# Performance work log

Hardware: AMD Instinct MI355X
Metric: run time of the kernel (lower is better)

Reference implementation:

```python
import jax, jax.numpy as jnp
import numpy as np

IN_CH = 12
STEP = 4
UPLAG = 2048
HIDDEN = 1024
OUTPUT = 256
BATCH = 2048
FEAT = UPLAG // STEP  # per-channel conv output length


def setup_inputs() -> dict:
    key = jax.random.key(0)
    ks = jax.random.split(key, 7)
    s = 1.0 / np.sqrt(STEP)
    x = jax.random.normal(ks[0], (BATCH, IN_CH, UPLAG), dtype=jnp.float32)
    # per-channel Conv1d(1,1,step,step) weights/biases, stacked: [C, step], [C]
    W1 = jax.random.uniform(ks[1], (IN_CH, STEP), jnp.float32, -s, s)
    b1 = jax.random.uniform(ks[2], (IN_CH,), jnp.float32, -s, s)
    d_in = IN_CH * FEAT
    s2 = 1.0 / np.sqrt(d_in)
    W2 = jax.random.uniform(ks[3], (d_in, HIDDEN), jnp.float32, -s2, s2)
    b2 = jax.random.uniform(ks[4], (HIDDEN,), jnp.float32, -s2, s2)
    s3 = 1.0 / np.sqrt(HIDDEN)
    W3 = jax.random.uniform(ks[5], (HIDDEN, OUTPUT), jnp.float32, -s3, s3)
    b3 = jax.random.uniform(ks[6], (OUTPUT,), jnp.float32, -s3, s3)
    return {"x": x, "W1": W1, "b1": b1, "W2": W2, "b2": b2, "W3": W3, "b3": b3}


def reference(x, W1, b1, W2, b2, W3, b3):
    B, C, L = x.shape
    # Non-overlapping patch reduction equivalent to Conv1d(1,1,step,step) per channel:
    # view [B, C, F, step], contract step dim against per-channel kernel.
    xp = x.reshape(B, C, L // STEP, STEP)
    conv = jnp.einsum('bcfk,ck->bcf', xp, W1) + b1[None, :, None]  # [B, C, F]
    flat = conv.reshape(B, C * (L // STEP))  # concat order: channel-major, matches torch.cat
    h = jax.nn.relu(flat @ W2 + b2)
    out = h @ W3 + b3
    return out.reshape(B, 1, -1)
```

## Files before the change

kernel.cpp:

```cpp
#include <hip/hip_runtime.h>
#include <hip/hip_bf16.h>

#define BATCH   2048
#define IN_CH   12
#define UPLAG   2048
#define STEP    4
#define FEAT    512
#define DIN     6144
#define HIDDEN  1024
#define OUTPUT  256

typedef __bf16 bf16x8 __attribute__((ext_vector_type(8)));
typedef float  f32x4  __attribute__((ext_vector_type(4)));

__device__ __forceinline__ unsigned short f2bf(float f) {
  unsigned int u = __builtin_bit_cast(unsigned int, f);
  unsigned int r = (u + 0x7fffu + ((u >> 16) & 1u)) >> 16;
  return (unsigned short)r;
}

__device__ __forceinline__ float bf2f(unsigned short h) {
  unsigned int u = ((unsigned int)h) << 16;
  return __builtin_bit_cast(float, u);
}

__device__ __forceinline__ void async_copy16(const unsigned short* g, unsigned short* l) {
  __builtin_amdgcn_global_load_lds(
      (const __attribute__((address_space(1))) unsigned int*)g,
      (__attribute__((address_space(3))) unsigned int*)l, 16, 0, 0);
}

__global__ __launch_bounds__(256) void conv_cast_kernel(
    const float* __restrict__ x, const float* __restrict__ W1,
    const float* __restrict__ b1, unsigned short* __restrict__ out)
{
  int gid = blockIdx.x * 256 + threadIdx.x;
  const int total = BATCH * DIN;
  if (gid >= total) return;
  int cf = gid % DIN;
  int c  = cf >> 9;
  float4 xv = ((const float4*)x)[gid];
  float4 wv = ((const float4*)W1)[c];
  float v = xv.x * wv.x + xv.y * wv.y + xv.z * wv.z + xv.w * wv.w + b1[c];
  out[gid] = f2bf(v);
}

__global__ __launch_bounds__(256) void transpose_cast(
    const float* __restrict__ in, unsigned short* __restrict__ out,
    int R, int Ncol)
{
  __shared__ float tile[32][33];
  int bx = blockIdx.x * 32;
  int by = blockIdx.y * 32;
  int tx = threadIdx.x, ty = threadIdx.y;
  #pragma unroll
  for (int i = 0; i < 32; i += 8)
    tile[ty + i][tx] = in[(size_t)(by + ty + i) * Ncol + bx + tx];
  __syncthreads();
  #pragma unroll
  for (int i = 0; i < 32; i += 8)
    out[(size_t)(bx + ty + i) * R + by + tx] = f2bf(tile[tx][ty + i]);
}

#define G1_BM 128
#define G1_BN 128
#define G1_BK 32
#define SPLITK 6

__global__ __launch_bounds__(256, 2) void gemm1_kernel(
    const unsigned short* __restrict__ A,
    const unsigned short* __restrict__ BT,
    unsigned short* __restrict__ Cp,
    int M, int N, int K)
{
  __shared__ unsigned short As[G1_BM * G1_BK];
  __shared__ unsigned short Bs[G1_BN * G1_BK];
  const int t    = threadIdx.x;
  const int lane = t & 63;
  const int wave = t >> 6;

  int b    = blockIdx.x;
  int xcdg = b & 7;
  int rest = b >> 3;
  int xt   = rest & 7;
  int zz   = rest >> 3;
  int zt   = zz >> 1;
  int yt   = (xcdg << 1) | (zz & 1);

  const int m0 = yt * G1_BM;
  const int n0 = xt * G1_BN;
  const int Ks = K / SPLITK;
  const int kbeg = zt * Ks;

  const int wm = (wave >> 1) * 64;
  const int wn = (wave & 1) * 64;
  const int lm = lane & 15;
  const int lk = (lane >> 4) * 8;

  f32x4 acc[4][4];
  #pragma unroll
  for (int i = 0; i < 4; i++)
    #pragma unroll
    for (int j = 0; j < 4; j++) {
      f32x4 z = {0.f, 0.f, 0.f, 0.f};
      acc[i][j] = z;
    }

  const unsigned short* Ag = A  + (size_t)m0 * K + kbeg;
  const unsigned short* Bg = BT + (size_t)n0 * K + kbeg;

  for (int kk = 0; kk < Ks; kk += G1_BK) {
    #pragma unroll
    for (int r = 0; r < 2; ++r) {
      int chunk = r * 256 + t;
      int row = chunk >> 2;
      int kc  = (chunk & 3) * 8;
      async_copy16(Ag + (size_t)row * K + kk + kc, As + chunk * 8);
    }
    #pragma unroll
    for (int r = 0; r < 2; ++r) {
      int chunk = r * 256 + t;
      int row = chunk >> 2;
      int kc  = (chunk & 3) * 8;
      async_copy16(Bg + (size_t)row * K + kk + kc, Bs + chunk * 8);
    }
    __syncthreads();

    bf16x8 af[4], bfr[4];
    #pragma unroll
    for (int i = 0; i < 4; i++)
      af[i] = *(const bf16x8*)(As + (wm + i * 16 + lm) * G1_BK + lk);
    #pragma unroll
    for (int j = 0; j < 4; j++)
      bfr[j] = *(const bf16x8*)(Bs + (wn + j * 16 + lm) * G1_BK + lk);
    #pragma unroll
    for (int i = 0; i < 4; i++)
      #pragma unroll
      for (int j = 0; j < 4; j++)
        acc[i][j] = __builtin_amdgcn_mfma_f32_16x16x32_bf16(af[i], bfr[j], acc[i][j], 0, 0, 0);
    __syncthreads();
  }

  unsigned short* Co = Cp + (size_t)zt * M * N;
  const int rbase = (lane >> 4) * 4;
  #pragma unroll
  for (int i = 0; i < 4; i++)
    #pragma unroll
    for (int j = 0; j < 4; j++) {
      int col = n0 + wn + j * 16 + lm;
      #pragma unroll
      for (int r = 0; r < 4; r++) {
        int row = m0 + wm + i * 16 + rbase + r;
        Co[(size_t)row * N + col] = f2bf(acc[i][j][r]);
      }
    }
}

__global__ __launch_bounds__(256) void reduce_bias_relu(
    const unsigned short* __restrict__ Cp, const float* __restrict__ b2,
    unsigned short* __restrict__ H)
{
  const int MN = BATCH * HIDDEN;
  int i4 = blockIdx.x * 256 + threadIdx.x;
  if (i4 >= MN / 4) return;
  float4 s = {0.f, 0.f, 0.f, 0.f};
  #pragma unroll
  for (int p = 0; p < SPLITK; ++p) {
    ushort4 a = ((const ushort4*)(Cp + (size_t)p * MN))[i4];
    s.x += bf2f(a.x); s.y += bf2f(a.y); s.z += bf2f(a.z); s.w += bf2f(a.w);
  }
  int col = (i4 * 4) & (HIDDEN - 1);
  float4 bb = *(const float4*)(b2 + col);
  ushort4 o;
  o.x = f2bf(fmaxf(s.x + bb.x, 0.f));
  o.y = f2bf(fmaxf(s.y + bb.y, 0.f));
  o.z = f2bf(fmaxf(s.z + bb.z, 0.f));
  o.w = f2bf(fmaxf(s.w + bb.w, 0.f));
  ((ushort4*)H)[i4] = o;
}

#define SPLITK2 4

__global__ __launch_bounds__(256, 2) void gemm2_kernel(
    const unsigned short* __restrict__ A,
    const unsigned short* __restrict__ BT,
    unsigned short* __restrict__ Cp)
{
  const int M = BATCH, N = OUTPUT, K = HIDDEN;
  __shared__ unsigned short As[64 * 32];
  __shared__ unsigned short Bs[64 * 32];
  const int t    = threadIdx.x;
  const int lane = t & 63;
  const int wave = t >> 6;
  const int m0 = blockIdx.y * 64;
  const int n0 = blockIdx.x * 64;
  const int Ks = K / SPLITK2;
  const int kbeg = blockIdx.z * Ks;
  const int wm = (wave >> 1) * 32;
  const int wn = (wave & 1) * 32;
  const int lm = lane & 15;
  const int lk = (lane >> 4) * 8;
  const int row = t >> 2;
  const int kc  = (t & 3) * 8;

  f32x4 acc[2][2];
  #pragma unroll
  for (int i = 0; i < 2; i++)
    #pragma unroll
    for (int j = 0; j < 2; j++) {
      f32x4 z = {0.f, 0.f, 0.f, 0.f};
      acc[i][j] = z;
    }

  const unsigned short* Ag = A  + (size_t)m0 * K + kbeg;
  const unsigned short* Bg = BT + (size_t)n0 * K + kbeg;

  for (int kk = 0; kk < Ks; kk += 32) {
    async_copy16(Ag + (size_t)row * K + kk + kc, As + t * 8);
    async_copy16(Bg + (size_t)row * K + kk + kc, Bs + t * 8);
    __syncthreads();
    bf16x8 af[2], bfr[2];
    #pragma unroll
    for (int i = 0; i < 2; i++)
      af[i] = *(const bf16x8*)(As + (wm + i * 16 + lm) * 32 + lk);
    #pragma unroll
    for (int j = 0; j < 2; j++)
      bfr[j] = *(const bf16x8*)(Bs + (wn + j * 16 + lm) * 32 + lk);
    #pragma unroll
    for (int i = 0; i < 2; i++)
      #pragma unroll
      for (int j = 0; j < 2; j++)
        acc[i][j] = __builtin_amdgcn_mfma_f32_16x16x32_bf16(af[i], bfr[j], acc[i][j], 0, 0, 0);
    __syncthreads();
  }

  unsigned short* Co = Cp + (size_t)blockIdx.z * M * N;
  const int rbase = (lane >> 4) * 4;
  #pragma unroll
  for (int i = 0; i < 2; i++)
    #pragma unroll
    for (int j = 0; j < 2; j++) {
      int col = n0 + wn + j * 16 + lm;
      #pragma unroll
      for (int r = 0; r < 4; r++) {
        int row_o = m0 + wm + i * 16 + rbase + r;
        Co[(size_t)row_o * N + col] = f2bf(acc[i][j][r]);
      }
    }
}

__global__ __launch_bounds__(256) void reduce2_bias(
    const unsigned short* __restrict__ Cp, const float* __restrict__ b3,
    float* __restrict__ out)
{
  const int MN = BATCH * OUTPUT;
  int i4 = blockIdx.x * 256 + threadIdx.x;
  if (i4 >= MN / 4) return;
  float4 s = {0.f, 0.f, 0.f, 0.f};
  #pragma unroll
  for (int p = 0; p < SPLITK2; ++p) {
    ushort4 a = ((const ushort4*)(Cp + (size_t)p * MN))[i4];
    s.x += bf2f(a.x); s.y += bf2f(a.y); s.z += bf2f(a.z); s.w += bf2f(a.w);
  }
  int col = (i4 * 4) & (OUTPUT - 1);
  float4 bb = *(const float4*)(b3 + col);
  float4 o = {s.x + bb.x, s.y + bb.y, s.z + bb.z, s.w + bb.w};
  ((float4*)out)[i4] = o;
}

extern "C" void kernel_launch(void* const* d_in, const int* in_sizes, int n_in,
                              void* d_out, int out_size, void* d_ws, size_t ws_size,
                              hipStream_t stream)
{
  const float* x  = (const float*)d_in[0];
  const float* W1 = (const float*)d_in[1];
  const float* b1 = (const float*)d_in[2];
  const float* W2 = (const float*)d_in[3];
  const float* b2 = (const float*)d_in[4];
  const float* W3 = (const float*)d_in[5];
  const float* b3 = (const float*)d_in[6];
  float* out = (float*)d_out;

  char* ws = (char*)d_ws;
  unsigned short* flatA = (unsigned short*)ws; ws += (size_t)BATCH * DIN * 2;
  unsigned short* W2T   = (unsigned short*)ws; ws += (size_t)HIDDEN * DIN * 2;
  unsigned short* W3T   = (unsigned short*)ws; ws += (size_t)OUTPUT * HIDDEN * 2;
  unsigned short* Cpart = (unsigned short*)ws; ws += (size_t)SPLITK * BATCH * HIDDEN * 2;
  unsigned short* H     = (unsigned short*)ws; ws += (size_t)BATCH * HIDDEN * 2;
  unsigned short* Cp2   = (unsigned short*)ws; ws += (size_t)SPLITK2 * BATCH * OUTPUT * 2;

  conv_cast_kernel<<<(BATCH * DIN) / 256, 256, 0, stream>>>(x, W1, b1, flatA);
  transpose_cast<<<dim3(HIDDEN / 32, DIN / 32), dim3(32, 8), 0, stream>>>(W2, W2T, DIN, HIDDEN);
  transpose_cast<<<dim3(OUTPUT / 32, HIDDEN / 32), dim3(32, 8), 0, stream>>>(W3, W3T, HIDDEN, OUTPUT);
  gemm1_kernel<<<768, 256, 0, stream>>>(flatA, W2T, Cpart, BATCH, HIDDEN, DIN);
  reduce_bias_relu<<<(BATCH * HIDDEN / 4) / 256, 256, 0, stream>>>(Cpart, b2, H);
  gemm2_kernel<<<dim3(OUTPUT / 64, BATCH / 64, SPLITK2), 256, 0, stream>>>(H, W3T, Cp2);
  reduce2_bias<<<(BATCH * OUTPUT / 4) / 256, 256, 0, stream>>>(Cp2, b3, out);
}
```

Baseline: 350.4 us.

## Fuse prep kernels and use swizzled BK=64 LDS tiles in both GEMMs

Merges the conv/cast and the two weight transpose-casts into one launch, with 64x64 transpose tiles. Both GEMMs double their K tile to 64 and store LDS rows with an XOR swizzle on 16-byte chunks, which halves the number of barrier pairs per K and is meant to cut LDS bank conflicts on fragment reads. LDS per block doubles, which may limit occupancy, and the fused prep kernel has grid-stride conv blocks alongside transpose blocks that use a 64x65 shared tile.

```diff
diff --git a/kernel.cpp b/kernel.cpp
--- a/kernel.cpp
+++ b/kernel.cpp
@@ -30,41 +30,56 @@
       (__attribute__((address_space(3))) unsigned int*)l, 16, 0, 0);
 }
 
-__global__ __launch_bounds__(256) void conv_cast_kernel(
+#define CONV_BLOCKS 4096
+#define W2T_BLOCKS  1536
+#define W3T_BLOCKS  64
+
+__global__ __launch_bounds__(256) void prep_kernel(
     const float* __restrict__ x, const float* __restrict__ W1,
-    const float* __restrict__ b1, unsigned short* __restrict__ out)
-{
-  int gid = blockIdx.x * 256 + threadIdx.x;
-  const int total = BATCH * DIN;
-  if (gid >= total) return;
-  int cf = gid % DIN;
-  int c  = cf >> 9;
-  float4 xv = ((const float4*)x)[gid];
-  float4 wv = ((const float4*)W1)[c];
-  float v = xv.x * wv.x + xv.y * wv.y + xv.z * wv.z + xv.w * wv.w + b1[c];
-  out[gid] = f2bf(v);
-}
-
-__global__ __launch_bounds__(256) void transpose_cast(
-    const float* __restrict__ in, unsigned short* __restrict__ out,
-    int R, int Ncol)
-{
-  __shared__ float tile[32][33];
-  int bx = blockIdx.x * 32;
-  int by = blockIdx.y * 32;
-  int tx = threadIdx.x, ty = threadIdx.y;
-  #pragma unroll
-  for (int i = 0; i < 32; i += 8)
+    const float* __restrict__ b1, unsigned short* __restrict__ flatA,
+    const float* __restrict__ W2, unsigned short* __restrict__ W2T,
+    const float* __restrict__ W3, unsigned short* __restrict__ W3T)
+{
+  __shared__ float tile[64][65];
+  const int t = threadIdx.x;
+  int b = blockIdx.x;
+
+  if (b < CONV_BLOCKS) {
+    const int total = BATCH * DIN;
+    for (int gid = b * 256 + t; gid < total; gid += CONV_BLOCKS * 256) {
+      int cf = gid % DIN;
+      int c  = cf >> 9;
+      float4 xv = ((const float4*)x)[gid];
+      float4 wv = ((const float4*)W1)[c];
+      float v = xv.x * wv.x + xv.y * wv.y + xv.z * wv.z + xv.w * wv.w + b1[c];
+      flatA[gid] = f2bf(v);
+    }
+    return;
+  }
+
+  const float* in; unsigned short* outp; int R, Ncol, bx, by;
+  if (b < CONV_BLOCKS + W2T_BLOCKS) {
+    int idx = b - CONV_BLOCKS;
+    in = W2; outp = W2T; R = DIN; Ncol = HIDDEN;
+    bx = (idx & 15) * 64; by = (idx >> 4) * 64;
+  } else {
+    int idx = b - CONV_BLOCKS - W2T_BLOCKS;
+    in = W3; outp = W3T; R = HIDDEN; Ncol = OUTPUT;
+    bx = (idx & 3) * 64; by = (idx >> 2) * 64;
+  }
+  int tx = t & 63, ty = t >> 6;
+  #pragma unroll
+  for (int i = 0; i < 64; i += 4)
     tile[ty + i][tx] = in[(size_t)(by + ty + i) * Ncol + bx + tx];
   __syncthreads();
   #pragma unroll
-  for (int i = 0; i < 32; i += 8)
-    out[(size_t)(bx + ty + i) * R + by + tx] = f2bf(tile[tx][ty + i]);
+  for (int i = 0; i < 64; i += 4)
+    outp[(size_t)(bx + ty + i) * R + by + tx] = f2bf(tile[tx][ty + i]);
 }
 
 #define G1_BM 128
 #define G1_BN 128
-#define G1_BK 32
+#define G1_BK 64
 #define SPLITK 6
 
 __global__ __launch_bounds__(256, 2) void gemm1_kernel(
@@ -95,7 +110,7 @@
   const int wm = (wave >> 1) * 64;
   const int wn = (wave & 1) * 64;
   const int lm = lane & 15;
-  const int lk = (lane >> 4) * 8;
+  const int kgrp = lane >> 4;
 
   f32x4 acc[4][4];
   #pragma unroll
@@ -111,38 +126,46 @@
 
   for (int kk = 0; kk < Ks; kk += G1_BK) {
     #pragma unroll
-    for (int r = 0; r < 2; ++r) {
-      int chunk = r * 256 + t;
-      int row = chunk >> 2;
-      int kc  = (chunk & 3) * 8;
-      async_copy16(Ag + (size_t)row * K + kk + kc, As + chunk * 8);
-    }
-    #pragma unroll
-    for (int r = 0; r < 2; ++r) {
-      int chunk = r * 256 + t;
-      int row = chunk >> 2;
-      int kc  = (chunk & 3) * 8;
-      async_copy16(Bg + (size_t)row * K + kk + kc, Bs + chunk * 8);
+    for (int r = 0; r < 4; ++r) {
+      int c = r * 256 + t;
+      int row = c >> 3;
+      int gk  = (c & 7) ^ (row & 7);
+      async_copy16(Ag + (size_t)row * K + kk + gk * 8, As + c * 8);
+    }
+    #pragma unroll
+    for (int r = 0; r < 4; ++r) {
+      int c = r * 256 + t;
+      int row = c >> 3;
+      int gk  = (c & 7) ^ (row & 7);
+      async_copy16(Bg + (size_t)row * K + kk + gk * 8, Bs + c * 8);
     }
     __syncthreads();
 
-    bf16x8 af[4], bfr[4];
-    #pragma unroll
-    for (int i = 0; i < 4; i++)
-      af[i] = *(const bf16x8*)(As + (wm + i * 16 + lm) * G1_BK + lk);
-    #pragma unroll
-    for (int j = 0; j < 4; j++)
-      bfr[j] = *(const bf16x8*)(Bs + (wn + j * 16 + lm) * G1_BK + lk);
-    #pragma unroll
-    for (int i = 0; i < 4; i++)
-      #pragma unroll
-      for (int j = 0; j < 4; j++)
-        acc[i][j] = __builtin_amdgcn_mfma_f32_16x16x32_bf16(af[i], bfr[j], acc[i][j], 0, 0, 0);
+    #pragma unroll
+    for (int s = 0; s < 2; ++s) {
+      const int kch = kgrp + s * 4;
+      bf16x8 af[4], bfr[4];
+      #pragma unroll
+      for (int i = 0; i < 4; i++) {
+        int row = wm + i * 16 + lm;
+        af[i] = *(const bf16x8*)(As + row * G1_BK + ((kch ^ (row & 7)) * 8));
+      }
+      #pragma unroll
+      for (int j = 0; j < 4; j++) {
+        int row = wn + j * 16 + lm;
+        bfr[j] = *(const bf16x8*)(Bs + row * G1_BK + ((kch ^ (row & 7)) * 8));
+      }
+      #pragma unroll
+      for (int i = 0; i < 4; i++)
+        #pragma unroll
+        for (int j = 0; j < 4; j++)
+          acc[i][j] = __builtin_amdgcn_mfma_f32_16x16x32_bf16(af[i], bfr[j], acc[i][j], 0, 0, 0);
+    }
     __syncthreads();
   }
 
   unsigned short* Co = Cp + (size_t)zt * M * N;
-  const int rbase = (lane >> 4) * 4;
+  const int rbase = kgrp * 4;
   #pragma unroll
   for (int i = 0; i < 4; i++)
     #pragma unroll
@@ -187,8 +210,8 @@
     unsigned short* __restrict__ Cp)
 {
   const int M = BATCH, N = OUTPUT, K = HIDDEN;
-  __shared__ unsigned short As[64 * 32];
-  __shared__ unsigned short Bs[64 * 32];
+  __shared__ unsigned short As[64 * 64];
+  __shared__ unsigned short Bs[64 * 64];
   const int t    = threadIdx.x;
   const int lane = t & 63;
   const int wave = t >> 6;
@@ -199,9 +222,7 @@
   const int wm = (wave >> 1) * 32;
   const int wn = (wave & 1) * 32;
   const int lm = lane & 15;
-  const int lk = (lane >> 4) * 8;
-  const int row = t >> 2;
-  const int kc  = (t & 3) * 8;
+  const int kgrp = lane >> 4;
 
   f32x4 acc[2][2];
   #pragma unroll
@@ -215,27 +236,48 @@
   const unsigned short* Ag = A  + (size_t)m0 * K + kbeg;
   const unsigned short* Bg = BT + (size_t)n0 * K + kbeg;
 
-  for (int kk = 0; kk < Ks; kk += 32) {
-    async_copy16(Ag + (size_t)row * K + kk + kc, As + t * 8);
-    async_copy16(Bg + (size_t)row * K + kk + kc, Bs + t * 8);
+  for (int kk = 0; kk < Ks; kk += 64) {
+    #pragma unroll
+    for (int r = 0; r < 2; ++r) {
+      int c = r * 256 + t;
+      int row = c >> 3;
+      int gk  = (c & 7) ^ (row & 7);
+      async_copy16(Ag + (size_t)row * K + kk + gk * 8, As + c * 8);
+    }
+    #pragma unroll
+    for (int r = 0; r < 2; ++r) {
+      int c = r * 256 + t;
+      int row = c >> 3;
+      int gk  = (c & 7) ^ (row & 7);
+      async_copy16(Bg + (size_t)row * K + kk + gk * 8, Bs + c * 8);
+    }
     __syncthreads();
-    bf16x8 af[2], bfr[2];
-    #pragma unroll
-    for (int i = 0; i < 2; i++)
-      af[i] = *(const bf16x8*)(As + (wm + i * 16 + lm) * 32 + lk);
-    #pragma unroll
-    for (int j = 0; j < 2; j++)
-      bfr[j] = *(const bf16x8*)(Bs + (wn + j * 16 + lm) * 32 + lk);
-    #pragma unroll
-    for (int i = 0; i < 2; i++)
-      #pragma unroll
-      for (int j = 0; j < 2; j++)
-        acc[i][j] = __builtin_amdgcn_mfma_f32_16x16x32_bf16(af[i], bfr[j], acc[i][j], 0, 0, 0);
+
+    #pragma unroll
+    for (int s = 0; s < 2; ++s) {
+      const int kch = kgrp + s * 4;
+      bf16x8 af[2], bfr[2];
+      #pragma unroll
+      for (int i = 0; i < 2; i++) {
+        int row = wm + i * 16 + lm;
+        af[i] = *(const bf16x8*)(As + row * 64 + ((kch ^ (row & 7)) * 8));
+      }
+      #pragma unroll
+      for (int j = 0; j < 2; j++) {
+        int row = wn + j * 16 + lm;
+        bfr[j] = *(const bf16x8*)(Bs + row * 64 + ((kch ^ (row & 7)) * 8));
+      }
+      #pragma unroll
+      for (int i = 0; i < 2; i++)
+        #pragma unroll
+        for (int j = 0; j < 2; j++)
+          acc[i][j] = __builtin_amdgcn_mfma_f32_16x16x32_bf16(af[i], bfr[j], acc[i][j], 0, 0, 0);
+    }
     __syncthreads();
   }
 
   unsigned short* Co = Cp + (size_t)blockIdx.z * M * N;
-  const int rbase = (lane >> 4) * 4;
+  const int rbase = kgrp * 4;
   #pragma unroll
   for (int i = 0; i < 2; i++)
     #pragma unroll
@@ -289,9 +331,8 @@
   unsigned short* H     = (unsigned short*)ws; ws += (size_t)BATCH * HIDDEN * 2;
   unsigned short* Cp2   = (unsigned short*)ws; ws += (size_t)SPLITK2 * BATCH * OUTPUT * 2;
 
-  conv_cast_kernel<<<(BATCH * DIN) / 256, 256, 0, stream>>>(x, W1, b1, flatA);
-  transpose_cast<<<dim3(HIDDEN / 32, DIN / 32), dim3(32, 8), 0, stream>>>(W2, W2T, DIN, HIDDEN);
-  transpose_cast<<<dim3(OUTPUT / 32, HIDDEN / 32), dim3(32, 8), 0, stream>>>(W3, W3T, HIDDEN, OUTPUT);
+  prep_kernel<<<CONV_BLOCKS + W2T_BLOCKS + W3T_BLOCKS, 256, 0, stream>>>(
+      x, W1, b1, flatA, W2, W2T, W3, W3T);
   gemm1_kernel<<<768, 256, 0, stream>>>(flatA, W2T, Cpart, BATCH, HIDDEN, DIN);
   reduce_bias_relu<<<(BATCH * HIDDEN / 4) / 256, 256, 0, stream>>>(Cpart, b2, H);
   gemm2_kernel<<<dim3(OUTPUT / 64, BATCH / 64, SPLITK2), 256, 0, stream>>>(H, W3T, Cp2);
```

Result: no change. 354.4 us (+1.1%).
